# Kernel optimization log

Measured on AMD Instinct MI355X. Metric: run time of the kernel, lower is better.

Reference implementation:

```python
import jax, jax.numpy as jnp
import numpy as np

DIM = 768
HEADS = 12
HIDDEN = 3072  # int(dim * 4.0)
EPS = 1e-5


def layernorm(x, g, b):
    mu = jnp.mean(x, axis=-1, keepdims=True)
    var = jnp.mean(jnp.square(x - mu), axis=-1, keepdims=True)
    return (x - mu) * jax.lax.rsqrt(var + EPS) * g + b


def setup_inputs() -> dict:
    key = jax.random.key(0)
    ks = jax.random.split(key, 8)
    s = 0.02
    return {
        "x": jax.random.normal(ks[0], (16, 1024, DIM), dtype=jnp.float32),
        "ln1_g": jnp.ones((DIM,), jnp.float32),
        "ln1_b": jnp.zeros((DIM,), jnp.float32),
        "qkv_w": jax.random.normal(ks[1], (3 * DIM, DIM), jnp.float32) * s,  # torch Linear weight [out,in], no bias (qkv_bias=False)
        "proj_w": jax.random.normal(ks[2], (DIM, DIM), jnp.float32) * s,
        "proj_b": jnp.zeros((DIM,), jnp.float32),
        "ln2_g": jnp.ones((DIM,), jnp.float32),
        "ln2_b": jnp.zeros((DIM,), jnp.float32),
        "fc1_w": jax.random.normal(ks[3], (HIDDEN, DIM), jnp.float32) * s,
        "fc1_b": jnp.zeros((HIDDEN,), jnp.float32),
        "fc2_w": jax.random.normal(ks[4], (DIM, HIDDEN), jnp.float32) * s,
        "fc2_b": jnp.zeros((DIM,), jnp.float32),
    }


def block(x, ln1_g, ln1_b, qkv_w, proj_w, proj_b, ln2_g, ln2_b, fc1_w, fc1_b, fc2_w, fc2_b):
    B, N, C = x.shape
    hd = C // HEADS
    scale = hd ** -0.5
    # --- attention branch ---
    h = layernorm(x, ln1_g, ln1_b)
    qkv = h @ qkv_w.T                                   # [B,N,3C]
    qkv = qkv.reshape(B, N, 3, HEADS, hd)
    q, k, v = jnp.moveaxis(qkv, 2, 0)                   # each [B,N,H,hd]
    q = q.transpose(0, 2, 1, 3)                          # [B,H,N,hd]
    k = k.transpose(0, 2, 1, 3)
    v = v.transpose(0, 2, 1, 3)
    attn = jnp.einsum('bhqd,bhkd->bhqk', q, k) * scale   # [B,H,N,N]
    attn = jax.nn.softmax(attn, axis=-1)
    o = jnp.einsum('bhqk,bhkd->bhqd', attn, v)           # [B,H,N,hd]
    o = o.transpose(0, 2, 1, 3).reshape(B, N, C)
    x = x + o @ proj_w.T + proj_b
    # --- mlp branch ---
    h = layernorm(x, ln2_g, ln2_b)
    h = jax.nn.gelu(h @ fc1_w.T + fc1_b, approximate=False)
    x = x + h @ fc2_w.T + fc2_b
    return x


def reference(x, ln1_g, ln1_b, qkv_w, proj_w, proj_b, ln2_g, ln2_b, fc1_w, fc1_b, fc2_w, fc2_b):
    return block(x, ln1_g, ln1_b, qkv_w, proj_w, proj_b, ln2_g, ln2_b, fc1_w, fc1_b, fc2_w, fc2_b)
```

## Files before the change

kernel.cpp:

```cpp
#include <hip/hip_runtime.h>
#include <cstdint>
#include <cstddef>

typedef __attribute__((ext_vector_type(8))) short short8;
typedef __attribute__((ext_vector_type(4))) float f32x4;
typedef __attribute__((ext_vector_type(4))) unsigned short us4;

#define GAS(p) ((const __attribute__((address_space(1))) void*)(p))
#define LAS(p) ((__attribute__((address_space(3))) void*)(p))

__device__ __forceinline__ unsigned short f2bf(float f) {
  union { float f; unsigned u; } v; v.f = f;
  return (unsigned short)((v.u + 0x7fffu + ((v.u >> 16) & 1u)) >> 16);
}

__global__ __launch_bounds__(256) void cvt_kernel(const float* __restrict__ in,
                                                  unsigned short* __restrict__ out, int n4) {
  int i = blockIdx.x * 256 + threadIdx.x;
  if (i >= n4) return;
  f32x4 v = ((const f32x4*)in)[i];
  us4 o;
#pragma unroll
  for (int j = 0; j < 4; ++j) o[j] = f2bf(v[j]);
  ((us4*)out)[i] = o;
}

__global__ __launch_bounds__(256) void ln_kernel(const float* __restrict__ x,
                                                 const float* __restrict__ g,
                                                 const float* __restrict__ b,
                                                 unsigned short* __restrict__ out) {
  const int wave = threadIdx.x >> 6, lane = threadIdx.x & 63;
  const int row = blockIdx.x * 4 + wave;
  const float* xr = x + (size_t)row * 768;
  f32x4 v[3];
  float s = 0.f, sq = 0.f;
#pragma unroll
  for (int c = 0; c < 3; ++c) {
    v[c] = *(const f32x4*)(xr + c * 256 + lane * 4);
#pragma unroll
    for (int j = 0; j < 4; ++j) { s += v[c][j]; sq += v[c][j] * v[c][j]; }
  }
#pragma unroll
  for (int off = 32; off > 0; off >>= 1) { s += __shfl_xor(s, off); sq += __shfl_xor(sq, off); }
  const float mu = s * (1.f / 768.f);
  const float var = sq * (1.f / 768.f) - mu * mu;
  const float rs = rsqrtf(var + 1e-5f);
  unsigned short* orow = out + (size_t)row * 768;
#pragma unroll
  for (int c = 0; c < 3; ++c) {
    f32x4 gg = *(const f32x4*)(g + c * 256 + lane * 4);
    f32x4 bb = *(const f32x4*)(b + c * 256 + lane * 4);
    us4 o;
#pragma unroll
    for (int j = 0; j < 4; ++j) o[j] = f2bf((v[c][j] - mu) * rs * gg[j] + bb[j]);
    *(us4*)(orow + c * 256 + lane * 4) = o;
  }
}

template <int EPI, int NN, int K>
__global__ __launch_bounds__(256) void gemm_bt(
    const unsigned short* __restrict__ A, const unsigned short* __restrict__ W,
    float* __restrict__ outF, const float* __restrict__ bias, const float* __restrict__ res,
    unsigned short* __restrict__ outU,
    unsigned short* __restrict__ q, unsigned short* __restrict__ kk, unsigned short* __restrict__ vt) {
  __shared__ unsigned short As[3][128 * 32];
  __shared__ unsigned short Bs[3][128 * 32];
  const int tid = threadIdx.x;
  const int wave = tid >> 6, lane = tid & 63;
  const int lr = lane & 15, lg = lane >> 4;
  const int wr = wave >> 1, wc = wave & 1;
  constexpr int GX = NN / 128;
  constexpr int NWG = GX * 128;
  int id = blockIdx.y * GX + blockIdx.x;
  id = (id & 7) * (NWG / 8) + (id >> 3);
  const int row0 = (id / GX) * 128, col0 = (id % GX) * 128;
  f32x4 acc[4][4] = {};
  const int sc = ((tid & 3) ^ ((tid >> 3) & 3)) * 8;
  const unsigned short* ag = A + (size_t)(row0 + (tid >> 2)) * K + sc;
  const unsigned short* bg = W + (size_t)(col0 + (tid >> 2)) * K + sc;
  const int rsw = (lg ^ ((lr >> 1) & 3)) << 4;
  const int KT = K / 32;
#define GEMM_STAGE(buf, kt_)                                                                   \
  {                                                                                            \
    const unsigned short* a0 = ag + (kt_) * 32;                                                \
    const unsigned short* b0 = bg + (kt_) * 32;                                                \
    __builtin_amdgcn_global_load_lds(GAS(a0), LAS(&As[buf][wave * 512]), 16, 0, 0);            \
    __builtin_amdgcn_global_load_lds(GAS(a0 + (size_t)64 * K), LAS(&As[buf][wave * 512 + 2048]), 16, 0, 0); \
    __builtin_amdgcn_global_load_lds(GAS(b0), LAS(&Bs[buf][wave * 512]), 16, 0, 0);            \
    __builtin_amdgcn_global_load_lds(GAS(b0 + (size_t)64 * K), LAS(&Bs[buf][wave * 512 + 2048]), 16, 0, 0); \
  }
  GEMM_STAGE(0, 0);
  GEMM_STAGE(1, 1);
  GEMM_STAGE(2, 2);
  int cur = 0;
  for (int kt = 0; kt < KT; ++kt) {
    if (kt < KT - 2)      asm volatile("s_waitcnt vmcnt(8)" ::: "memory");
    else if (kt < KT - 1) asm volatile("s_waitcnt vmcnt(4)" ::: "memory");
    else                  asm volatile("s_waitcnt vmcnt(0)" ::: "memory");
    __builtin_amdgcn_s_barrier();
    __builtin_amdgcn_sched_barrier(0);
    short8 af[4], bfv[4];
#pragma unroll
    for (int m = 0; m < 4; ++m)
      af[m] = *(const short8*)((const char*)&As[cur][0] + (wr * 64 + m * 16 + lr) * 64 + rsw);
#pragma unroll
    for (int n = 0; n < 4; ++n)
      bfv[n] = *(const short8*)((const char*)&Bs[cur][0] + (wc * 64 + n * 16 + lr) * 64 + rsw);
    asm volatile("s_waitcnt lgkmcnt(0)" ::: "memory");
    __builtin_amdgcn_sched_barrier(0);
    __builtin_amdgcn_s_barrier();
    if (kt + 3 < KT + 0) {
      if (kt + 3 <= KT - 1) GEMM_STAGE(cur, kt + 3);
    }
#pragma unroll
    for (int m = 0; m < 4; ++m)
#pragma unroll
      for (int n = 0; n < 4; ++n)
        acc[m][n] = __builtin_amdgcn_mfma_f32_16x16x32_bf16(af[m], bfv[n], acc[m][n], 0, 0, 0);
    cur = (cur == 2) ? 0 : cur + 1;
  }
#undef GEMM_STAGE
#pragma unroll
  for (int m = 0; m < 4; ++m)
#pragma unroll
    for (int n = 0; n < 4; ++n)
#pragma unroll
      for (int r = 0; r < 4; ++r) {
        const int grow = row0 + wr * 64 + m * 16 + lg * 4 + r;
        const int gcol = col0 + wc * 64 + n * 16 + lr;
        const float val = acc[m][n][r];
        if (EPI == 0) {
          const int s = gcol / 768;
          const int rem = gcol - s * 768;
          const int hh = rem >> 6, d = rem & 63;
          const int bt = grow >> 10, nt = grow & 1023;
          const size_t bh = (size_t)(bt * 12 + hh);
          if (s == 0)      q[(bh * 1024 + nt) * 64 + d] = f2bf(val * 0.125f);
          else if (s == 1) kk[(bh * 1024 + nt) * 64 + d] = f2bf(val);
          else             vt[(bh * 64 + d) * 1024 + nt] = f2bf(val);
        } else if (EPI == 1) {
          const size_t idx = (size_t)grow * NN + gcol;
          outF[idx] = val + bias[gcol] + res[idx];
        } else {
          const size_t idx = (size_t)grow * NN + gcol;
          const float t = val + bias[gcol];
          float u = 0.7978845608f * (t + 0.044715f * t * t * t);
          u = fminf(fmaxf(u, -10.f), 10.f);
          const float e = __expf(2.f * u);
          const float th = (e - 1.f) / (e + 1.f);
          outU[idx] = f2bf(0.5f * t * (1.f + th));
        }
      }
}

__global__ __launch_bounds__(256) void attn_kernel(
    const unsigned short* __restrict__ Q, const unsigned short* __restrict__ K,
    const unsigned short* __restrict__ V, unsigned short* __restrict__ O) {
  __shared__ unsigned short Ks[2][64 * 64];
  __shared__ unsigned short Vs[2][64 * 64];
  const int tid = threadIdx.x, wave = tid >> 6, lane = tid & 63;
  const int lr = lane & 15, lg = lane >> 4;
  const int qt = blockIdx.x, hh = blockIdx.y, bb = blockIdx.z;
  const size_t bh = (size_t)bb * 12 + hh;
  const unsigned short* Qg = Q + bh * 1024 * 64;
  const unsigned short* Kg = K + bh * 1024 * 64;
  const unsigned short* Vg = V + bh * 64 * 1024;
  const int q0 = qt * 128 + wave * 32;
  short8 aq[2][2];
#pragma unroll
  for (int nq = 0; nq < 2; ++nq)
#pragma unroll
    for (int kb = 0; kb < 2; ++kb)
      aq[nq][kb] = *(const short8*)(Qg + (size_t)(q0 + nq * 16 + lr) * 64 + kb * 32 + lg * 8);
  float m_run[2] = {-1e30f, -1e30f}, l_run[2] = {0.f, 0.f};
  f32x4 oacc[4][2] = {};
  const int srow = tid >> 3;
  const int sswz = (((tid & 7) * 16) ^ ((srow & 7) << 4)) >> 1;
  const int srcLo = (lane & 15) | ((lane & 16) << 1);
  const int srcHi = srcLo + 16;
  const bool hiSel = lg >= 2;
#define ATTN_STAGE(buf, t_)                                                                      \
  {                                                                                              \
    const int kv_ = (t_) * 64;                                                                   \
    _Pragma("unroll")                                                                            \
    for (int is = 0; is < 2; ++is) {                                                             \
      __builtin_amdgcn_global_load_lds(GAS(Kg + (size_t)(kv_ + is * 32 + srow) * 64 + sswz),     \
                                       LAS(&Ks[buf][is * 2048 + wave * 512]), 16, 0, 0);         \
      __builtin_amdgcn_global_load_lds(GAS(Vg + (size_t)(is * 32 + srow) * 1024 + kv_ + sswz),   \
                                       LAS(&Vs[buf][is * 2048 + wave * 512]), 16, 0, 0);         \
    }                                                                                            \
  }
  ATTN_STAGE(0, 0);
  ATTN_STAGE(1, 1);
  for (int t = 0; t < 16; ++t) {
    const int cur = t & 1;
    if (t < 15) asm volatile("s_waitcnt vmcnt(4)" ::: "memory");
    else        asm volatile("s_waitcnt vmcnt(0)" ::: "memory");
    __builtin_amdgcn_s_barrier();
    __builtin_amdgcn_sched_barrier(0);
    f32x4 sacc[4][2] = {};
#pragma unroll
    for (int kb = 0; kb < 2; ++kb) {
      short8 kf[4];
#pragma unroll
      for (int mk = 0; mk < 4; ++mk) {
        const int row = mk * 16 + lr;
        const int boff = row * 128 + ((kb * 64 + lg * 16) ^ ((row & 7) << 4));
        kf[mk] = *(const short8*)((const char*)&Ks[cur][0] + boff);
      }
#pragma unroll
      for (int mk = 0; mk < 4; ++mk)
#pragma unroll
        for (int nq = 0; nq < 2; ++nq)
          sacc[mk][nq] = __builtin_amdgcn_mfma_f32_16x16x32_bf16(kf[mk], aq[nq][kb], sacc[mk][nq], 0, 0, 0);
    }
    unsigned pk[4][2][2];
#pragma unroll
    for (int nq = 0; nq < 2; ++nq) {
      float mx = sacc[0][nq][0];
#pragma unroll
      for (int mk = 0; mk < 4; ++mk)
#pragma unroll
        for (int r = 0; r < 4; ++r) mx = fmaxf(mx, sacc[mk][nq][r]);
      mx = fmaxf(mx, __shfl_xor(mx, 16));
      mx = fmaxf(mx, __shfl_xor(mx, 32));
      const float mnew = fmaxf(m_run[nq], mx);
      const float alpha = __expf(m_run[nq] - mnew);
      float ssum = 0.f;
#pragma unroll
      for (int mk = 0; mk < 4; ++mk)
#pragma unroll
        for (int r = 0; r < 4; ++r) {
          const float p = __expf(sacc[mk][nq][r] - mnew);
          sacc[mk][nq][r] = p;
          ssum += p;
        }
      ssum += __shfl_xor(ssum, 16);
      ssum += __shfl_xor(ssum, 32);
      l_run[nq] = alpha * l_run[nq] + ssum;
      m_run[nq] = mnew;
#pragma unroll
      for (int mb = 0; mb < 4; ++mb)
#pragma unroll
        for (int r = 0; r < 4; ++r) oacc[mb][nq][r] *= alpha;
#pragma unroll
      for (int mk = 0; mk < 4; ++mk) {
        asm("v_cvt_pk_bf16_f32 %0, %1, %2" : "=v"(pk[mk][nq][0]) : "v"(sacc[mk][nq][0]), "v"(sacc[mk][nq][1]));
        asm("v_cvt_pk_bf16_f32 %0, %1, %2" : "=v"(pk[mk][nq][1]) : "v"(sacc[mk][nq][2]), "v"(sacc[mk][nq][3]));
      }
    }
#pragma unroll
    for (int kb = 0; kb < 2; ++kb) {
      short8 vf[4];
#pragma unroll
      for (int mb = 0; mb < 4; ++mb) {
        const int row = mb * 16 + lr;
        const int boff = row * 128 + ((kb * 64 + lg * 16) ^ ((row & 7) << 4));
        vf[mb] = *(const short8*)((const char*)&Vs[cur][0] + boff);
      }
#pragma unroll
      for (int nq = 0; nq < 2; ++nq) {
        unsigned a0 = (unsigned)__shfl((int)pk[2 * kb][nq][0], srcLo);
        unsigned b0 = (unsigned)__shfl((int)pk[2 * kb + 1][nq][0], srcLo);
        unsigned a1 = (unsigned)__shfl((int)pk[2 * kb][nq][1], srcLo);
        unsigned b1 = (unsigned)__shfl((int)pk[2 * kb + 1][nq][1], srcLo);
        unsigned a2 = (unsigned)__shfl((int)pk[2 * kb][nq][0], srcHi);
        unsigned b2 = (unsigned)__shfl((int)pk[2 * kb + 1][nq][0], srcHi);
        unsigned a3 = (unsigned)__shfl((int)pk[2 * kb][nq][1], srcHi);
        unsigned b3 = (unsigned)__shfl((int)pk[2 * kb + 1][nq][1], srcHi);
        union { unsigned u[4]; short8 s; } cvt;
        cvt.u[0] = hiSel ? b0 : a0;
        cvt.u[1] = hiSel ? b1 : a1;
        cvt.u[2] = hiSel ? b2 : a2;
        cvt.u[3] = hiSel ? b3 : a3;
        const short8 pb = cvt.s;
#pragma unroll
        for (int mb = 0; mb < 4; ++mb)
          oacc[mb][nq] = __builtin_amdgcn_mfma_f32_16x16x32_bf16(vf[mb], pb, oacc[mb][nq], 0, 0, 0);
      }
    }
    asm volatile("s_waitcnt lgkmcnt(0)" ::: "memory");
    __builtin_amdgcn_sched_barrier(0);
    __builtin_amdgcn_s_barrier();
    if (t + 2 < 16) ATTN_STAGE(cur, t + 2);
  }
#undef ATTN_STAGE
#pragma unroll
  for (int nq = 0; nq < 2; ++nq) {
    const float linv = 1.f / l_run[nq];
    const size_t tok = (size_t)(bb << 10) + q0 + nq * 16 + lr;
#pragma unroll
    for (int mb = 0; mb < 4; ++mb) {
      us4 o;
#pragma unroll
      for (int r = 0; r < 4; ++r) o[r] = f2bf(oacc[mb][nq][r] * linv);
      *(us4*)(O + tok * 768 + hh * 64 + mb * 16 + lg * 4) = o;
    }
  }
}

extern "C" void kernel_launch(void* const* d_in, const int* in_sizes, int n_in,
                              void* d_out, int out_size, void* d_ws, size_t ws_size,
                              hipStream_t stream) {
  const float* x      = (const float*)d_in[0];
  const float* ln1_g  = (const float*)d_in[1];
  const float* ln1_b  = (const float*)d_in[2];
  const float* qkv_w  = (const float*)d_in[3];
  const float* proj_w = (const float*)d_in[4];
  const float* proj_b = (const float*)d_in[5];
  const float* ln2_g  = (const float*)d_in[6];
  const float* ln2_b  = (const float*)d_in[7];
  const float* fc1_w  = (const float*)d_in[8];
  const float* fc1_b  = (const float*)d_in[9];
  const float* fc2_w  = (const float*)d_in[10];
  const float* fc2_b  = (const float*)d_in[11];
  float* out = (float*)d_out;
  char* ws = (char*)d_ws;

  unsigned short* wqkv = (unsigned short*)(ws + 0);
  unsigned short* wproj = (unsigned short*)(ws + 3538944);
  unsigned short* wfc1 = (unsigned short*)(ws + 4718592);
  unsigned short* wfc2 = (unsigned short*)(ws + 9437184);
  unsigned short* hbuf = (unsigned short*)(ws + 14155776);
  char* big = ws + 39321600;
  unsigned short* qb  = (unsigned short*)(big);
  unsigned short* kb  = (unsigned short*)(big + 25165824);
  unsigned short* vtb = (unsigned short*)(big + 50331648);
  unsigned short* ob  = (unsigned short*)(big + 75497472);
  unsigned short* hid = (unsigned short*)(big);

  cvt_kernel<<<1728, 256, 0, stream>>>(qkv_w, wqkv, 442368);
  cvt_kernel<<<576, 256, 0, stream>>>(proj_w, wproj, 147456);
  cvt_kernel<<<2304, 256, 0, stream>>>(fc1_w, wfc1, 589824);
  cvt_kernel<<<2304, 256, 0, stream>>>(fc2_w, wfc2, 589824);

  ln_kernel<<<4096, 256, 0, stream>>>(x, ln1_g, ln1_b, hbuf);
  gemm_bt<0, 2304, 768><<<dim3(18, 128), 256, 0, stream>>>(
      hbuf, wqkv, nullptr, nullptr, nullptr, nullptr, qb, kb, vtb);
  attn_kernel<<<dim3(8, 12, 16), 256, 0, stream>>>(qb, kb, vtb, ob);
  gemm_bt<1, 768, 768><<<dim3(6, 128), 256, 0, stream>>>(
      ob, wproj, out, proj_b, x, nullptr, nullptr, nullptr, nullptr);
  ln_kernel<<<4096, 256, 0, stream>>>(out, ln2_g, ln2_b, hbuf);
  gemm_bt<2, 3072, 768><<<dim3(24, 128), 256, 0, stream>>>(
      hbuf, wfc1, nullptr, fc1_b, nullptr, hid, nullptr, nullptr, nullptr);
  gemm_bt<1, 768, 3072><<<dim3(6, 128), 256, 0, stream>>>(
      hid, wfc2, out, fc2_b, out, nullptr, nullptr, nullptr, nullptr);
}
```

Before: 527.0 us.

## Enlarge GEMM tiles to 256x256 with 512 threads and unrolled triple-buffer loop

```diff
diff --git a/kernel.cpp b/kernel.cpp
--- a/kernel.cpp
+++ b/kernel.cpp
@@ -58,75 +58,86 @@
 }
 
 template <int EPI, int NN, int K>
-__global__ __launch_bounds__(256) void gemm_bt(
+__global__ __launch_bounds__(512, 2) void gemm256(
     const unsigned short* __restrict__ A, const unsigned short* __restrict__ W,
     float* __restrict__ outF, const float* __restrict__ bias, const float* __restrict__ res,
     unsigned short* __restrict__ outU,
     unsigned short* __restrict__ q, unsigned short* __restrict__ kk, unsigned short* __restrict__ vt) {
-  __shared__ unsigned short As[3][128 * 32];
-  __shared__ unsigned short Bs[3][128 * 32];
+  __shared__ unsigned short As[3][8192];
+  __shared__ unsigned short Bs[3][8192];
   const int tid = threadIdx.x;
   const int wave = tid >> 6, lane = tid & 63;
   const int lr = lane & 15, lg = lane >> 4;
-  const int wr = wave >> 1, wc = wave & 1;
-  constexpr int GX = NN / 128;
-  constexpr int NWG = GX * 128;
+  const int wr = wave >> 2, wc = wave & 3;
+  constexpr int GX = NN / 256;
+  constexpr int NWG = GX * 64;
   int id = blockIdx.y * GX + blockIdx.x;
   id = (id & 7) * (NWG / 8) + (id >> 3);
-  const int row0 = (id / GX) * 128, col0 = (id % GX) * 128;
-  f32x4 acc[4][4] = {};
+  const int row0 = (id / GX) * 256, col0 = (id % GX) * 256;
+  f32x4 acc[8][4] = {};
   const int sc = ((tid & 3) ^ ((tid >> 3) & 3)) * 8;
   const unsigned short* ag = A + (size_t)(row0 + (tid >> 2)) * K + sc;
   const unsigned short* bg = W + (size_t)(col0 + (tid >> 2)) * K + sc;
   const int rsw = (lg ^ ((lr >> 1) & 3)) << 4;
   const int KT = K / 32;
-#define GEMM_STAGE(buf, kt_)                                                                   \
-  {                                                                                            \
-    const unsigned short* a0 = ag + (kt_) * 32;                                                \
-    const unsigned short* b0 = bg + (kt_) * 32;                                                \
-    __builtin_amdgcn_global_load_lds(GAS(a0), LAS(&As[buf][wave * 512]), 16, 0, 0);            \
-    __builtin_amdgcn_global_load_lds(GAS(a0 + (size_t)64 * K), LAS(&As[buf][wave * 512 + 2048]), 16, 0, 0); \
-    __builtin_amdgcn_global_load_lds(GAS(b0), LAS(&Bs[buf][wave * 512]), 16, 0, 0);            \
-    __builtin_amdgcn_global_load_lds(GAS(b0 + (size_t)64 * K), LAS(&Bs[buf][wave * 512 + 2048]), 16, 0, 0); \
-  }
-  GEMM_STAGE(0, 0);
-  GEMM_STAGE(1, 1);
-  GEMM_STAGE(2, 2);
-  int cur = 0;
-  for (int kt = 0; kt < KT; ++kt) {
-    if (kt < KT - 2)      asm volatile("s_waitcnt vmcnt(8)" ::: "memory");
-    else if (kt < KT - 1) asm volatile("s_waitcnt vmcnt(4)" ::: "memory");
-    else                  asm volatile("s_waitcnt vmcnt(0)" ::: "memory");
-    __builtin_amdgcn_s_barrier();
-    __builtin_amdgcn_sched_barrier(0);
-    short8 af[4], bfv[4];
-#pragma unroll
-    for (int m = 0; m < 4; ++m)
-      af[m] = *(const short8*)((const char*)&As[cur][0] + (wr * 64 + m * 16 + lr) * 64 + rsw);
+
+#define STG(buf, kt_)                                                                              \
+  {                                                                                                \
+    const unsigned short* a0 = ag + (kt_) * 32;                                                    \
+    const unsigned short* b0 = bg + (kt_) * 32;                                                    \
+    __builtin_amdgcn_global_load_lds(GAS(a0), LAS(&As[buf][wave * 512]), 16, 0, 0);                \
+    __builtin_amdgcn_global_load_lds(GAS(a0 + (size_t)128 * K), LAS(&As[buf][4096 + wave * 512]), 16, 0, 0); \
+    __builtin_amdgcn_global_load_lds(GAS(b0), LAS(&Bs[buf][wave * 512]), 16, 0, 0);                \
+    __builtin_amdgcn_global_load_lds(GAS(b0 + (size_t)128 * K), LAS(&Bs[buf][4096 + wave * 512]), 16, 0, 0); \
+  }
+
+#define KSTEP(cur, vm, dostage, kt_)                                                               \
+  {                                                                                                \
+    asm volatile("s_waitcnt vmcnt(" #vm ")" ::: "memory");                                         \
+    __builtin_amdgcn_s_barrier();                                                                  \
+    __builtin_amdgcn_sched_barrier(0);                                                             \
+    short8 af[8], bfv[4];                                                                          \
+    _Pragma("unroll")                                                                              \
+    for (int m = 0; m < 8; ++m)                                                                    \
+      af[m] = *(const short8*)((const char*)&As[cur][0] + (wr * 128 + m * 16 + lr) * 64 + rsw);    \
+    _Pragma("unroll")                                                                              \
+    for (int n = 0; n < 4; ++n)                                                                    \
+      bfv[n] = *(const short8*)((const char*)&Bs[cur][0] + (wc * 64 + n * 16 + lr) * 64 + rsw);    \
+    asm volatile("s_waitcnt lgkmcnt(0)" ::: "memory");                                             \
+    __builtin_amdgcn_sched_barrier(0);                                                             \
+    __builtin_amdgcn_s_barrier();                                                                  \
+    if (dostage) STG(cur, kt_);                                                                    \
+    __builtin_amdgcn_s_setprio(1);                                                                 \
+    _Pragma("unroll")                                                                              \
+    for (int m = 0; m < 8; ++m)                                                                    \
+      _Pragma("unroll")                                                                            \
+      for (int n = 0; n < 4; ++n)                                                                  \
+        acc[m][n] = __builtin_amdgcn_mfma_f32_16x16x32_bf16(af[m], bfv[n], acc[m][n], 0, 0, 0);    \
+    __builtin_amdgcn_s_setprio(0);                                                                 \
+  }
+
+  STG(0, 0);
+  STG(1, 1);
+  STG(2, 2);
+  for (int u = 0; u < KT / 3 - 1; ++u) {
+    const int k3 = u * 3;
+    KSTEP(0, 8, true, k3 + 3);
+    KSTEP(1, 8, true, k3 + 4);
+    KSTEP(2, 8, true, k3 + 5);
+  }
+  KSTEP(0, 8, false, 0);
+  KSTEP(1, 4, false, 0);
+  KSTEP(2, 0, false, 0);
+#undef KSTEP
+#undef STG
+
+#pragma unroll
+  for (int m = 0; m < 8; ++m)
 #pragma unroll
     for (int n = 0; n < 4; ++n)
-      bfv[n] = *(const short8*)((const char*)&Bs[cur][0] + (wc * 64 + n * 16 + lr) * 64 + rsw);
-    asm volatile("s_waitcnt lgkmcnt(0)" ::: "memory");
-    __builtin_amdgcn_sched_barrier(0);
-    __builtin_amdgcn_s_barrier();
-    if (kt + 3 < KT + 0) {
-      if (kt + 3 <= KT - 1) GEMM_STAGE(cur, kt + 3);
-    }
-#pragma unroll
-    for (int m = 0; m < 4; ++m)
-#pragma unroll
-      for (int n = 0; n < 4; ++n)
-        acc[m][n] = __builtin_amdgcn_mfma_f32_16x16x32_bf16(af[m], bfv[n], acc[m][n], 0, 0, 0);
-    cur = (cur == 2) ? 0 : cur + 1;
-  }
-#undef GEMM_STAGE
-#pragma unroll
-  for (int m = 0; m < 4; ++m)
-#pragma unroll
-    for (int n = 0; n < 4; ++n)
 #pragma unroll
       for (int r = 0; r < 4; ++r) {
-        const int grow = row0 + wr * 64 + m * 16 + lg * 4 + r;
+        const int grow = row0 + wr * 128 + m * 16 + lg * 4 + r;
         const int gcol = col0 + wc * 64 + n * 16 + lr;
         const float val = acc[m][n][r];
         if (EPI == 0) {
@@ -335,14 +346,14 @@
   cvt_kernel<<<2304, 256, 0, stream>>>(fc2_w, wfc2, 589824);
 
   ln_kernel<<<4096, 256, 0, stream>>>(x, ln1_g, ln1_b, hbuf);
-  gemm_bt<0, 2304, 768><<<dim3(18, 128), 256, 0, stream>>>(
+  gemm256<0, 2304, 768><<<dim3(9, 64), 512, 0, stream>>>(
       hbuf, wqkv, nullptr, nullptr, nullptr, nullptr, qb, kb, vtb);
   attn_kernel<<<dim3(8, 12, 16), 256, 0, stream>>>(qb, kb, vtb, ob);
-  gemm_bt<1, 768, 768><<<dim3(6, 128), 256, 0, stream>>>(
+  gemm256<1, 768, 768><<<dim3(3, 64), 512, 0, stream>>>(
       ob, wproj, out, proj_b, x, nullptr, nullptr, nullptr, nullptr);
   ln_kernel<<<4096, 256, 0, stream>>>(out, ln2_g, ln2_b, hbuf);
-  gemm_bt<2, 3072, 768><<<dim3(24, 128), 256, 0, stream>>>(
+  gemm256<2, 3072, 768><<<dim3(12, 64), 512, 0, stream>>>(
       hbuf, wfc1, nullptr, fc1_b, nullptr, hid, nullptr, nullptr, nullptr);
-  gemm_bt<1, 768, 3072><<<dim3(6, 128), 256, 0, stream>>>(
+  gemm256<1, 768, 3072><<<dim3(3, 64), 512, 0, stream>>>(
       hid, wfc2, out, fc2_b, out, nullptr, nullptr, nullptr, nullptr);
 }
```

Result: slower. 565.8 us (+7.4%).
